# Kernel tuning notes

Measured on AMD Instinct MI355X. Metric: run time of the kernel, lower is better.

The kernel has to match this reference:

```python
import jax, jax.numpy as jnp
import numpy as np

N_QUBITS = 12
FAST_DEPTH = 4
FAST_DECAY = 0.9
LATENT = 512
BATCH = 2048


def _apply_ry(state, theta, wire):
    # state: (B, 2**n) real; RY is a real rotation. PennyLane default.qubit:
    # wire 0 is the most-significant bit of the state index.
    B = state.shape[0]
    s = state.reshape(B, 1 << wire, 2, -1)
    h = theta * 0.5
    c = jnp.cos(h)[:, None, None]
    sn = jnp.sin(h)[:, None, None]
    s0, s1 = s[:, :, 0], s[:, :, 1]
    out = jnp.stack([c * s0 - sn * s1, sn * s0 + c * s1], axis=2)
    return out.reshape(state.shape)


def _apply_cnot_adjacent(state, wire):
    # CNOT with control=wire, target=wire+1 (nearest-neighbor chain)
    B = state.shape[0]
    s = state.reshape(B, 1 << wire, 2, 2, -1)
    out = jnp.stack([s[:, :, 0], s[:, :, 1, ::-1]], axis=2)
    return out.reshape(state.shape)


def _fwp_circuit(x, fast, n_qubits, n_outputs):
    # x: (B, n_qubits) RY encoding angles; fast: (B, depth, n_qubits)
    B = x.shape[0]
    dim = 1 << n_qubits
    # Hadamard layer on |0...0> -> uniform positive real amplitudes.
    state = jnp.full((B, dim), 2.0 ** (-n_qubits / 2), dtype=x.dtype)
    for w in range(n_qubits):
        state = _apply_ry(state, x[:, w], w)
    for layer in range(fast.shape[1]):
        for w in range(n_qubits - 1):
            state = _apply_cnot_adjacent(state, w)
        for w in range(n_qubits):
            state = _apply_ry(state, fast[:, layer, w], w)
    probs = state * state  # real state -> |amp|^2
    outs = []
    for w in range(n_outputs):
        p = probs.reshape(B, 1 << w, 2, -1)
        outs.append(p[:, :, 0].sum(axis=(1, 2)) - p[:, :, 1].sum(axis=(1, 2)))
    return jnp.stack(outs, axis=1)  # (B, n_outputs) PauliZ expvals


def setup_inputs() -> dict:
    key = jax.random.key(0)
    ks = jax.random.split(key, 6)
    n, depth, latent = N_QUBITS, FAST_DEPTH, LATENT
    return {
        "x_t": jax.random.normal(ks[0], (BATCH, n), jnp.float32),
        "fast_prev": jax.random.normal(ks[1], (BATCH, depth, n), jnp.float32) * 0.1,
        "W_enc": jax.random.normal(ks[2], (latent, n), jnp.float32) / np.sqrt(n).astype(np.float32),
        "b_enc": jnp.zeros((latent,), jnp.float32),
        "W_upd": jax.random.normal(ks[3], (depth * n, latent), jnp.float32) / np.sqrt(latent).astype(np.float32),
        "b_upd": jnp.zeros((depth * n,), jnp.float32),
        "W_ro": jax.random.normal(ks[4], (1, n), jnp.float32) / np.sqrt(n).astype(np.float32),
        "b_ro": jnp.zeros((1,), jnp.float32),
    }


def reference(x_t, fast_prev, W_enc, b_enc, W_upd, b_upd, W_ro, b_ro):
    latent = jnp.tanh(x_t @ W_enc.T + b_enc)
    delta = (latent @ W_upd.T + b_upd).reshape(x_t.shape[0], FAST_DEPTH, N_QUBITS)
    fast_next = FAST_DECAY * fast_prev + delta
    q_out = _fwp_circuit(x_t, fast_next, N_QUBITS, N_QUBITS)  # n_outputs = n_qubits
    y_t = q_out @ W_ro.T + b_ro
    return (y_t, fast_next)
```

## Files before the change

### kernel.cpp

```cpp
#include <hip/hip_runtime.h>

static constexpr int NQ    = 12;
static constexpr int DEPTH = 4;
static constexpr int LAT   = 512;
static constexpr int FAST  = DEPTH * NQ;
static constexpr float DECAY = 0.9f;
static constexpr int PITCH = 65;


template<int S>
__device__ __forceinline__ void bfly(float (&v)[64], float c, float s) {
    #pragma unroll
    for (int r0 = 0; r0 < 64; r0++) {
        if ((r0 & S) == 0) {
            float a = v[r0], b = v[r0 + S];
            v[r0]     = c * a - s * b;
            v[r0 + S] = s * a + c * b;
        }
    }
}

template<int K>
__device__ __forceinline__ void ry6(float (&v)[64], const float* lc, const float* ls) {
    if constexpr (K < 6) {
        bfly<(1 << (5 - K))>(v, lc[K], ls[K]);
        ry6<K + 1>(v, lc, ls);
    }
}

__global__ __launch_bounds__(64, 2)
void fwp_kernel(const float* __restrict__ x_t,
                const float* __restrict__ fast_prev,
                const float* __restrict__ W_enc,
                const float* __restrict__ b_enc,
                const float* __restrict__ W_upd,
                const float* __restrict__ b_upd,
                const float* __restrict__ W_ro,
                const float* __restrict__ b_ro,
                float* __restrict__ out_y,
                float* __restrict__ out_fast) {
    const int lane = threadIdx.x;
    const int b    = blockIdx.x;

    __shared__ __align__(16) float s_xch[64 * PITCH];
    __shared__ float s_c[FAST], s_s[FAST];

    float* s_lat = s_xch;

    float xr = (lane < NQ) ? x_t[b * NQ + lane] : 0.0f;
    float xa[NQ];
    #pragma unroll
    for (int k = 0; k < NQ; k++) xa[k] = __shfl(xr, k, 64);

    #pragma unroll
    for (int t = 0; t < LAT / 64; t++) {
        int j = lane + 64 * t;
        const float4* wr = (const float4*)(W_enc + j * NQ);
        float4 a0 = wr[0], a1 = wr[1], a2 = wr[2];
        float sum = b_enc[j]
            + a0.x * xa[0] + a0.y * xa[1] + a0.z * xa[2]  + a0.w * xa[3]
            + a1.x * xa[4] + a1.y * xa[5] + a1.z * xa[6]  + a1.w * xa[7]
            + a2.x * xa[8] + a2.y * xa[9] + a2.z * xa[10] + a2.w * xa[11];
        s_lat[j] = tanhf(sum);
    }
    __syncthreads();

    if (lane < FAST) {
        const float4* wr = (const float4*)(W_upd + lane * LAT);
        const float4* lr = (const float4*)(s_lat);
        float sum = b_upd[lane];
        #pragma unroll 16
        for (int j = 0; j < LAT / 4; j++) {
            float4 w4 = wr[j];
            float4 l4 = lr[j];
            sum += w4.x * l4.x + w4.y * l4.y + w4.z * l4.z + w4.w * l4.w;
        }
        float ang = DECAY * fast_prev[b * FAST + lane] + sum;
        out_fast[b * FAST + lane] = ang;
        float hh = 0.5f * ang;
        s_c[lane] = __cosf(hh);
        s_s[lane] = __sinf(hh);
    }
    __syncthreads();

    float g0[NQ], g1[NQ];
    #pragma unroll
    for (int w = 0; w < NQ; w++) {
        float hh = 0.5f * xa[w];
        float c = __cosf(hh), s = __sinf(hh);
        g0[w] = (c - s) * 0.70710678118654752f;
        g1[w] = (c + s) * 0.70710678118654752f;
    }
    float L = 1.0f;
    #pragma unroll
    for (int w = 0; w < 6; w++)
        L *= ((lane >> (5 - w)) & 1) ? g1[w] : g0[w];

    float v[64];
    v[0] = L;
    #pragma unroll
    for (int w = 6; w < NQ; w++) {
        const int S = 1 << (11 - w);
        #pragma unroll
        for (int r = 0; r < 64; r += 2 * S) {
            v[r + S] = v[r] * g1[w];
            v[r]     = v[r] * g0[w];
        }
    }

    const int A0 = ((lane ^ (lane >> 1)) & 31) | (lane & 32);
    const int A1 = A0 ^ 32;

    #pragma unroll 1
    for (int layer = 0; layer < DEPTH; layer++) {
        const float* lc = &s_c[layer * NQ];
        const float* ls = &s_s[layer * NQ];

        __syncthreads();
        #pragma unroll
        for (int r = 0; r < 64; r++) s_xch[lane * PITCH + r] = v[r];
        __syncthreads();
        #pragma unroll
        for (int r = 0; r < 64; r++) {
            const int g = r ^ (r >> 1);
            v[r] = s_xch[g * PITCH + ((r & 1) ? A1 : A0)];
        }
        ry6<0>(v, lc, ls);

        __syncthreads();
        #pragma unroll
        for (int r = 0; r < 64; r++) s_xch[lane * PITCH + r] = v[r];
        __syncthreads();
        #pragma unroll
        for (int r = 0; r < 64; r++) v[r] = s_xch[r * PITCH + lane];
        ry6<0>(v, lc + 6, ls + 6);
    }

    float tot = 0.0f, pw[6] = {0, 0, 0, 0, 0, 0};
    #pragma unroll
    for (int r = 0; r < 64; r++) {
        float p = v[r] * v[r];
        tot += p;
        pw[0] += (r & 32) ? -p : p;
        pw[1] += (r & 16) ? -p : p;
        pw[2] += (r & 8)  ? -p : p;
        pw[3] += (r & 4)  ? -p : p;
        pw[4] += (r & 2)  ? -p : p;
        pw[5] += (r & 1)  ? -p : p;
    }
    float sl = 0.0f;
    #pragma unroll
    for (int w = 0; w < 6; w++) {
        float c = W_ro[w];
        sl += ((lane >> (5 - w)) & 1) ? -c : c;
    }
    float y = sl * tot;
    #pragma unroll
    for (int k = 0; k < 6; k++) y += W_ro[6 + k] * pw[k];
    #pragma unroll
    for (int m = 32; m >= 1; m >>= 1) y += __shfl_xor(y, m, 64);
    if (lane == 0) out_y[b] = y + b_ro[0];
}

extern "C" void kernel_launch(void* const* d_in, const int* in_sizes, int n_in,
                              void* d_out, int out_size, void* d_ws, size_t ws_size,
                              hipStream_t stream) {
    const float* x_t       = (const float*)d_in[0];
    const float* fast_prev = (const float*)d_in[1];
    const float* W_enc     = (const float*)d_in[2];
    const float* b_enc     = (const float*)d_in[3];
    const float* W_upd     = (const float*)d_in[4];
    const float* b_upd     = (const float*)d_in[5];
    const float* W_ro      = (const float*)d_in[6];
    const float* b_ro      = (const float*)d_in[7];
    float* out = (float*)d_out;

    fwp_kernel<<<2048, 64, 0, stream>>>(x_t, fast_prev, W_enc, b_enc,
                                        W_upd, b_upd, W_ro, b_ro,
                                        out , out + 2048 );
}
```

Before: 115.1 us.

## Use packed-FP32 butterflies, wave-level fences, and vectorized LDS stores

The RY butterflies are rewritten on 2-wide float vectors so the compiler can emit packed FP32 math. Because each block is a single 64-lane wave, the __syncthreads calls are replaced with block thread fences and wave barriers. The LDS exchange now writes float2 with PITCH raised to 66 for 8-byte alignment, and the layer loop is fully unrolled with the angles preloaded into registers. The risks are LDS bank conflicts from the new pitch, higher register pressure from unrolling, and relying on the one-wave-per-block assumption for correct ordering.

```diff
diff --git a/kernel.cpp b/kernel.cpp
--- a/kernel.cpp
+++ b/kernel.cpp
@@ -5,27 +5,49 @@
 static constexpr int LAT   = 512;
 static constexpr int FAST  = DEPTH * NQ;
 static constexpr float DECAY = 0.9f;
-static constexpr int PITCH = 65;
-
+static constexpr int PITCH = 66;
+
+using v2f = __attribute__((ext_vector_type(2))) float;
+
+
+#define RAW_FENCE() __threadfence_block()
+#define WAR_FENCE() __builtin_amdgcn_wave_barrier()
 
 template<int S>
-__device__ __forceinline__ void bfly(float (&v)[64], float c, float s) {
-    #pragma unroll
-    for (int r0 = 0; r0 < 64; r0++) {
+__device__ __forceinline__ void bfly2(float (&v)[64], float c, float s) {
+    v2f c2 = {c, c}, s2 = {s, s};
+    #pragma unroll
+    for (int r0 = 0; r0 < 64; r0 += 2) {
         if ((r0 & S) == 0) {
-            float a = v[r0], b = v[r0 + S];
-            v[r0]     = c * a - s * b;
-            v[r0 + S] = s * a + c * b;
-        }
-    }
-}
-
-template<int K>
+            v2f a = {v[r0],     v[r0 + 1]};
+            v2f b = {v[r0 + S], v[r0 + S + 1]};
+            v2f na = c2 * a - s2 * b;
+            v2f nb = s2 * a + c2 * b;
+            v[r0]         = na.x;  v[r0 + 1]     = na.y;
+            v[r0 + S]     = nb.x;  v[r0 + S + 1] = nb.y;
+        }
+    }
+}
+
+__device__ __forceinline__ void bfly1(float (&v)[64], float c, float s) {
+    v2f cs = {c, s}, nsc = {-s, c};
+    #pragma unroll
+    for (int r0 = 0; r0 < 64; r0 += 2) {
+        float a = v[r0], b = v[r0 + 1];
+        v2f aa = {a, a}, bb = {b, b};
+        v2f res = cs * aa + nsc * bb;
+        v[r0]     = res.x;
+        v[r0 + 1] = res.y;
+    }
+}
+
 __device__ __forceinline__ void ry6(float (&v)[64], const float* lc, const float* ls) {
-    if constexpr (K < 6) {
-        bfly<(1 << (5 - K))>(v, lc[K], ls[K]);
-        ry6<K + 1>(v, lc, ls);
-    }
+    bfly2<32>(v, lc[0], ls[0]);
+    bfly2<16>(v, lc[1], ls[1]);
+    bfly2<8>(v, lc[2], ls[2]);
+    bfly2<4>(v, lc[3], ls[3]);
+    bfly2<2>(v, lc[4], ls[4]);
+    bfly1(v, lc[5], ls[5]);
 }
 
 __global__ __launch_bounds__(64, 2)
@@ -63,7 +85,7 @@
             + a2.x * xa[8] + a2.y * xa[9] + a2.z * xa[10] + a2.w * xa[11];
         s_lat[j] = tanhf(sum);
     }
-    __syncthreads();
+    RAW_FENCE();
 
     if (lane < FAST) {
         const float4* wr = (const float4*)(W_upd + lane * LAT);
@@ -81,7 +103,7 @@
         s_c[lane] = __cosf(hh);
         s_s[lane] = __sinf(hh);
     }
-    __syncthreads();
+    RAW_FENCE();
 
     float g0[NQ], g1[NQ];
     #pragma unroll
@@ -111,29 +133,35 @@
     const int A0 = ((lane ^ (lane >> 1)) & 31) | (lane & 32);
     const int A1 = A0 ^ 32;
 
-    #pragma unroll 1
+    #pragma unroll
     for (int layer = 0; layer < DEPTH; layer++) {
-        const float* lc = &s_c[layer * NQ];
-        const float* ls = &s_s[layer * NQ];
-
-        __syncthreads();
-        #pragma unroll
-        for (int r = 0; r < 64; r++) s_xch[lane * PITCH + r] = v[r];
-        __syncthreads();
+        float lc[NQ], ls[NQ];
+        #pragma unroll
+        for (int w = 0; w < NQ; w++) {
+            lc[w] = s_c[layer * NQ + w];
+            ls[w] = s_s[layer * NQ + w];
+        }
+
+        WAR_FENCE();
+        #pragma unroll
+        for (int k = 0; k < 32; k++)
+            *(v2f*)&s_xch[lane * PITCH + 2 * k] = (v2f){v[2 * k], v[2 * k + 1]};
+        RAW_FENCE();
         #pragma unroll
         for (int r = 0; r < 64; r++) {
             const int g = r ^ (r >> 1);
             v[r] = s_xch[g * PITCH + ((r & 1) ? A1 : A0)];
         }
-        ry6<0>(v, lc, ls);
-
-        __syncthreads();
-        #pragma unroll
-        for (int r = 0; r < 64; r++) s_xch[lane * PITCH + r] = v[r];
-        __syncthreads();
+        ry6(v, lc, ls);
+
+        WAR_FENCE();
+        #pragma unroll
+        for (int k = 0; k < 32; k++)
+            *(v2f*)&s_xch[lane * PITCH + 2 * k] = (v2f){v[2 * k], v[2 * k + 1]};
+        RAW_FENCE();
         #pragma unroll
         for (int r = 0; r < 64; r++) v[r] = s_xch[r * PITCH + lane];
-        ry6<0>(v, lc + 6, ls + 6);
+        ry6(v, lc + 6, ls + 6);
     }
 
     float tot = 0.0f, pw[6] = {0, 0, 0, 0, 0, 0};
```

New measurement: 111.3 us. -3.4%, faster.
